# Optimization experiments

Hardware: AMD Instinct MI355X
Metric: run time of the kernel (lower is better)

## Reference

```python
import jax, jax.numpy as jnp
import numpy as np

B, N, E_PER_G = 32, 2048, 16384
NF, NHID, NCLS = 128, 128, 10
RATIO = 0.5
NT = B * N
E = B * E_PER_G
K1 = int(np.ceil(RATIO * N))        # 1024 nodes kept per graph after pool1
K2 = int(np.ceil(RATIO * K1))       # 512
K3 = int(np.ceil(RATIO * K2))       # 256


def setup_inputs() -> dict:
    key = jax.random.key(0)
    ks = jax.random.split(key, 16)
    x = jax.random.normal(ks[0], (NT, NF), dtype=jnp.float32)
    off = (jnp.arange(B, dtype=jnp.int32) * N)[:, None]
    src = (jax.random.randint(ks[1], (B, E_PER_G), 0, N, dtype=jnp.int32) + off).reshape(-1)
    dst = (jax.random.randint(ks[2], (B, E_PER_G), 0, N, dtype=jnp.int32) + off).reshape(-1)
    edge_index = jnp.stack([src, dst])
    batch = jnp.repeat(jnp.arange(B, dtype=jnp.int32), N)
    def lin(k, i, o):
        return jax.random.normal(k, (i, o), jnp.float32) / np.float32(np.sqrt(i))
    return {
        'x': x, 'edge_index': edge_index, 'batch': batch,
        'W1': lin(ks[3], NF, NHID), 'b1': jnp.zeros((NHID,), jnp.float32),
        'Wp1': lin(ks[4], NHID, 1), 'bp1': jnp.zeros((1,), jnp.float32),
        'W2': lin(ks[5], NHID, NHID), 'b2': jnp.zeros((NHID,), jnp.float32),
        'Wp2': lin(ks[6], NHID, 1), 'bp2': jnp.zeros((1,), jnp.float32),
        'W3': lin(ks[7], NHID, NHID), 'b3': jnp.zeros((NHID,), jnp.float32),
        'Wp3': lin(ks[8], NHID, 1), 'bp3': jnp.zeros((1,), jnp.float32),
        'lin1_W': lin(ks[9], 2 * NHID, NHID), 'lin1_b': jnp.zeros((NHID,), jnp.float32),
        'lin2_W': lin(ks[10], NHID, NHID // 2), 'lin2_b': jnp.zeros((NHID // 2,), jnp.float32),
        'lin3_W': lin(ks[11], NHID // 2, NCLS), 'lin3_b': jnp.zeros((NCLS,), jnp.float32),
    }


def gcn(x, src, dst, emask, nmask, W, b):
    # PyG GCNConv: add self-loops, symmetric normalization D^-1/2 (A+I) D^-1/2 @ (x W) + b.
    # Removed nodes/edges carry weight 0 via masks (equivalent to filter_adj re-indexing).
    h = x @ W
    deg = jnp.zeros((NT,), h.dtype).at[dst].add(emask) + nmask
    dinv = jnp.where(deg > 0, 1.0, 0.0) * jax.lax.rsqrt(jnp.where(deg > 0, deg, 1.0))
    coef = dinv[src] * dinv[dst] * emask               # [E]
    out = jnp.zeros_like(h).at[dst].add(coef[:, None] * h[src])
    out = out + ((dinv * dinv) * nmask)[:, None] * h   # self-loop term, norm = 1/deg
    return out + b


def sagpool(x, src, dst, emask, nmask, Wp, bp, k):
    # score = GCNConv(nhid,1); keep top-k per graph; x <- x[perm] * tanh(score[perm])
    score = gcn(x, src, dst, emask, nmask, Wp, bp)[:, 0]          # [NT]
    s = jnp.where(nmask > 0, score, -jnp.inf).reshape(B, N)
    _, idx = jax.lax.top_k(s, k)                                   # [B, k]
    keep = jnp.zeros((B, N), x.dtype).at[jnp.arange(B)[:, None], idx].set(1.0).reshape(-1)
    x_new = x * jnp.tanh(score)[:, None] * keep[:, None]
    emask_new = emask * keep[src] * keep[dst]                      # filter_adj
    return x_new, emask_new, keep


def readout(x, nmask, count):
    # [global_max_pool, global_mean_pool] over active nodes of each graph
    xb = x.reshape(B, N, -1)
    m = nmask.reshape(B, N, 1)
    mx = jnp.max(jnp.where(m > 0, xb, -jnp.inf), axis=1)
    mn = jnp.sum(xb * m, axis=1) / count
    return jnp.concatenate([mx, mn], axis=-1)


def reference(x, edge_index, batch, W1, b1, Wp1, bp1, W2, b2, Wp2, bp2,
              W3, b3, Wp3, bp3, lin1_W, lin1_b, lin2_W, lin2_b, lin3_W, lin3_b):
    src, dst = edge_index[0], edge_index[1]
    emask = jnp.ones((E,), x.dtype)
    nmask = jnp.ones((NT,), x.dtype)

    h = jax.nn.relu(gcn(x, src, dst, emask, nmask, W1, b1))
    h, emask, nmask = sagpool(h, src, dst, emask, nmask, Wp1, bp1, K1)
    x1 = readout(h, nmask, jnp.asarray(K1, x.dtype))

    h = jax.nn.relu(gcn(h, src, dst, emask, nmask, W2, b2))
    h, emask, nmask = sagpool(h, src, dst, emask, nmask, Wp2, bp2, K2)
    x2 = readout(h, nmask, jnp.asarray(K2, x.dtype))

    h = jax.nn.relu(gcn(h, src, dst, emask, nmask, W3, b3))
    h, emask, nmask = sagpool(h, src, dst, emask, nmask, Wp3, bp3, K3)
    x3 = readout(h, nmask, jnp.asarray(K3, x.dtype))

    g = x1 + x2 + x3
    g = jax.nn.relu(g @ lin1_W + lin1_b)   # dropout = identity in eval
    g = jax.nn.relu(g @ lin2_W + lin2_b)
    return jax.nn.log_softmax(g @ lin3_W + lin3_b, axis=-1)
```

## Files before the change

kernel.cpp:

```cpp
#include <hip/hip_runtime.h>
#include <math.h>


namespace {

constexpr int B_  = 32;
constexpr int N_  = 2048;
constexpr int NT  = B_ * N_;
constexpr int EPG = 16384;
constexpr int E_  = B_ * EPG;
constexpr int NCLS = 10;
constexpr int AST = 132;

__device__ __forceinline__ int relabel(int bid, int bpgsh) {
  int x = bid & 7, slot = bid >> 3;
  int g = x + 8 * (slot >> bpgsh);
  return (g << bpgsh) + (slot & ((1 << bpgsh) - 1));
}

__device__ void csr_build(const int* __restrict__ src, const int* __restrict__ dst,
                          int* __restrict__ off, int* __restrict__ srcp,
                          float* __restrict__ dinv, float* __restrict__ ds,
                          float* __restrict__ sws, int* hist) {
  const int g = blockIdx.x;
  const int t = threadIdx.x;
  const int base_n = g * N_;
  const int base_e = g * EPG;
  int* wsum4 = hist + 2048;
#pragma unroll
  for (int i = 0; i < 8; ++i) hist[t + 256 * i] = 0;
  __syncthreads();
  for (int i = 0; i < EPG / 256; i += 8) {
    int dd[8];
#pragma unroll
    for (int j = 0; j < 8; ++j) dd[j] = dst[base_e + t + 256 * (i + j)];
#pragma unroll
    for (int j = 0; j < 8; ++j) atomicAdd(&hist[dd[j] - base_n], 1);
  }
  __syncthreads();
  int a[8], ssum = 0;
#pragma unroll
  for (int i = 0; i < 8; ++i) { a[i] = hist[8 * t + i]; ssum += a[i]; }
  {
    int lane = t & 63, w = t >> 6;
    int v = ssum;
#pragma unroll
    for (int o = 1; o < 64; o <<= 1) {
      int nv = __shfl_up(v, o);
      if (lane >= o) v += nv;
    }
    if (lane == 63) wsum4[w] = v;
    __syncthreads();
    if (t == 0) {
      int accv = 0;
      for (int i = 0; i < 4; ++i) { int tmp = wsum4[i]; wsum4[i] = accv; accv += tmp; }
    }
    __syncthreads();
    int run = wsum4[w] + v - ssum;
#pragma unroll
    for (int i = 0; i < 8; ++i) {
      int n = 8 * t + i;
      off[base_n + n] = base_e + run;
      hist[n] = run;
      float d0 = 1.f + (float)a[i];
      float di0 = 1.f / sqrtf(d0);
      dinv[base_n + n] = di0;
      ds[base_n + n] = di0;
      sws[base_n + n] = di0 * di0;
      run += a[i];
    }
    if (g == B_ - 1 && t == 0) off[NT] = E_;
  }
  __syncthreads();
  for (int i = 0; i < EPG / 256; i += 8) {
    int dd[8], ss[8];
#pragma unroll
    for (int j = 0; j < 8; ++j) {
      int e = base_e + t + 256 * (i + j);
      dd[j] = dst[e];
      ss[j] = src[e];
    }
#pragma unroll
    for (int j = 0; j < 8; ++j) {
      int slot = atomicAdd(&hist[dd[j] - base_n], 1);
      srcp[base_e + slot] = ss[j];
    }
  }
}

__global__ __launch_bounds__(256) void k_matmul(const float* __restrict__ A,
                                                const float* __restrict__ W,
                                                float* __restrict__ C,
                                                const int* __restrict__ kept,
                                                int kshift, int bpgsh,
                                                const float* __restrict__ scaleArr,
                                                float* __restrict__ pmx,
                                                float* __restrict__ psm,
                                                const int* __restrict__ src,
                                                const int* __restrict__ dst,
                                                int* __restrict__ off,
                                                int* __restrict__ srcp,
                                                float* __restrict__ dinvW,
                                                float* __restrict__ dsW,
                                                float* __restrict__ swsW,
                                                int csrBlocks) {
  __shared__ float Ast[2][32 * AST];
  __shared__ float Ws[2][32 * 128];
  __shared__ int rowid[128];
  __shared__ float rsc[128];
  if ((int)blockIdx.x < csrBlocks) {
    csr_build(src, dst, off, srcp, dinvW, dsW, swsW, (int*)&Ast[0][0]);
    return;
  }
  const int tid = threadIdx.x;
  const int tile = relabel((int)blockIdx.x - csrBlocks, bpgsh);
  if (kept) {
    if (tid < 128) {
      int q = tile * 128 + tid;
      int g = q >> kshift;
      int row = kept[g * N_ + (q - (g << kshift))];
      rowid[tid] = row;
      rsc[tid] = scaleArr[row];
    }
    __syncthreads();
  }
  const int rowq = tid >> 4;
  const int colq = tid & 15;
  float4 va[4], vw[4];
#pragma unroll
  for (int i = 0; i < 4; ++i) {
    int idx = tid + 256 * i;
    int row = idx >> 3, f4 = idx & 7;
    int grw = kept ? rowid[row] : tile * 128 + row;
    va[i] = *(const float4*)&A[(size_t)grw * 128 + 4 * f4];
  }
#pragma unroll
  for (int i = 0; i < 4; ++i) {
    int idx = tid + 256 * i;
    int kk = idx >> 5, cf = idx & 31;
    vw[i] = *(const float4*)&W[(size_t)kk * 128 + 4 * cf];
  }
#pragma unroll
  for (int i = 0; i < 4; ++i) {
    int idx = tid + 256 * i;
    int row = idx >> 3, f4 = idx & 7;
    Ast[0][(4 * f4 + 0) * AST + row] = va[i].x;
    Ast[0][(4 * f4 + 1) * AST + row] = va[i].y;
    Ast[0][(4 * f4 + 2) * AST + row] = va[i].z;
    Ast[0][(4 * f4 + 3) * AST + row] = va[i].w;
  }
#pragma unroll
  for (int i = 0; i < 4; ++i) {
    int idx = tid + 256 * i;
    int kk = idx >> 5, cf = idx & 31;
    *(float4*)&Ws[0][kk * 128 + 4 * cf] = vw[i];
  }
  __syncthreads();
  float acc[8][8] = {};
  for (int c = 0; c < 4; ++c) {
    int cur = c & 1;
    if (c < 3) {
      int k0n = 32 * (c + 1);
#pragma unroll
      for (int i = 0; i < 4; ++i) {
        int idx = tid + 256 * i;
        int row = idx >> 3, f4 = idx & 7;
        int grw = kept ? rowid[row] : tile * 128 + row;
        va[i] = *(const float4*)&A[(size_t)grw * 128 + k0n + 4 * f4];
      }
#pragma unroll
      for (int i = 0; i < 4; ++i) {
        int idx = tid + 256 * i;
        int kk = idx >> 5, cf = idx & 31;
        vw[i] = *(const float4*)&W[(size_t)(k0n + kk) * 128 + 4 * cf];
      }
    }
#pragma unroll 2
    for (int kk = 0; kk < 32; ++kk) {
      float4 a0 = *(const float4*)&Ast[cur][kk * AST + 8 * rowq];
      float4 a1 = *(const float4*)&Ast[cur][kk * AST + 8 * rowq + 4];
      float4 w0 = *(const float4*)&Ws[cur][kk * 128 + 4 * colq];
      float4 w1 = *(const float4*)&Ws[cur][kk * 128 + 64 + 4 * colq];
      float a[8] = {a0.x, a0.y, a0.z, a0.w, a1.x, a1.y, a1.z, a1.w};
      float w[8] = {w0.x, w0.y, w0.z, w0.w, w1.x, w1.y, w1.z, w1.w};
#pragma unroll
      for (int r = 0; r < 8; ++r)
#pragma unroll
        for (int cc = 0; cc < 8; ++cc) acc[r][cc] += a[r] * w[cc];
    }
    if (kept) {
      int kkf = tid >> 3;
      int r0 = (tid & 7) * 16;
      float mxv = -INFINITY, smv = 0.f;
#pragma unroll
      for (int rr = 0; rr < 16; rr += 4) {
        float4 av = *(const float4*)&Ast[cur][kkf * AST + r0 + rr];
        float4 s4 = *(const float4*)&rsc[r0 + rr];
        float v0 = av.x * s4.x, v1 = av.y * s4.y;
        float v2 = av.z * s4.z, v3 = av.w * s4.w;
        mxv = fmaxf(fmaxf(fmaxf(mxv, v0), fmaxf(v1, v2)), v3);
        smv += v0 + v1 + v2 + v3;
      }
#pragma unroll
      for (int o = 4; o >= 1; o >>= 1) {
        mxv = fmaxf(mxv, __shfl_down(mxv, o));
        smv += __shfl_down(smv, o);
      }
      if ((tid & 7) == 0) {
        pmx[(size_t)tile * 128 + 32 * c + kkf] = mxv;
        psm[(size_t)tile * 128 + 32 * c + kkf] = smv;
      }
    }
    if (c < 3) {
      int nxt = cur ^ 1;
#pragma unroll
      for (int i = 0; i < 4; ++i) {
        int idx = tid + 256 * i;
        int row = idx >> 3, f4 = idx & 7;
        Ast[nxt][(4 * f4 + 0) * AST + row] = va[i].x;
        Ast[nxt][(4 * f4 + 1) * AST + row] = va[i].y;
        Ast[nxt][(4 * f4 + 2) * AST + row] = va[i].z;
        Ast[nxt][(4 * f4 + 3) * AST + row] = va[i].w;
      }
#pragma unroll
      for (int i = 0; i < 4; ++i) {
        int idx = tid + 256 * i;
        int kk = idx >> 5, cf = idx & 31;
        *(float4*)&Ws[nxt][kk * 128 + 4 * cf] = vw[i];
      }
      __syncthreads();
    }
  }
#pragma unroll
  for (int r = 0; r < 8; ++r) {
    int grw = kept ? rowid[8 * rowq + r] : tile * 128 + 8 * rowq + r;
    float* Crow = &C[(size_t)grw * 128];
    *(float4*)&Crow[4 * colq] = make_float4(acc[r][0], acc[r][1], acc[r][2], acc[r][3]);
    *(float4*)&Crow[64 + 4 * colq] = make_float4(acc[r][4], acc[r][5], acc[r][6], acc[r][7]);
  }
}

__global__ __launch_bounds__(256) void k_agg(const float4* __restrict__ t4,
                                             const int* __restrict__ off,
                                             const int* __restrict__ srcp,
                                             const float* __restrict__ dinv,
                                             const float* __restrict__ ds,
                                             const float* __restrict__ sws,
                                             const float* __restrict__ bias,
                                             const float* __restrict__ Wp,
                                             float4* __restrict__ h4,
                                             float* __restrict__ t1,
                                             const int* __restrict__ kept,
                                             int kshift, int bpgsh) {
  int q = relabel(blockIdx.x, bpgsh) * 8 + (threadIdx.x >> 5);
  int node;
  if (kept) {
    int g = q >> kshift;
    node = kept[g * N_ + (q - (g << kshift))];
  } else {
    node = q;
  }
  const int lane = threadIdx.x & 31;
  const float dvi = dinv[node];
  float sw = sws[node];
  float4 self = t4[(size_t)node * 32 + lane];
  float4 acc = make_float4(sw * self.x, sw * self.y, sw * self.z, sw * self.w);
  int s = off[node], en = off[node + 1];
  int j = s;
  for (; j + 8 <= en; j += 8) {
    int sv[8];
    float cv[8];
#pragma unroll
    for (int i = 0; i < 8; ++i) sv[i] = srcp[j + i];
#pragma unroll
    for (int i = 0; i < 8; ++i) cv[i] = ds[sv[i]] * dvi;
#pragma unroll
    for (int i = 0; i < 8; ++i) {
      if (cv[i] != 0.f) {
        float4 r = t4[(size_t)sv[i] * 32 + lane];
        acc.x += cv[i] * r.x; acc.y += cv[i] * r.y;
        acc.z += cv[i] * r.z; acc.w += cv[i] * r.w;
      }
    }
  }
  for (; j < en; ++j) {
    int s0 = srcp[j];
    float c0 = ds[s0] * dvi;
    if (c0 != 0.f) {
      float4 r0 = t4[(size_t)s0 * 32 + lane];
      acc.x += c0 * r0.x; acc.y += c0 * r0.y; acc.z += c0 * r0.z; acc.w += c0 * r0.w;
    }
  }
  float4 b4 = ((const float4*)bias)[lane];
  acc.x = fmaxf(acc.x + b4.x, 0.f);
  acc.y = fmaxf(acc.y + b4.y, 0.f);
  acc.z = fmaxf(acc.z + b4.z, 0.f);
  acc.w = fmaxf(acc.w + b4.w, 0.f);
  h4[(size_t)node * 32 + lane] = acc;
  float4 wp = ((const float4*)Wp)[lane];
  float part = acc.x * wp.x + acc.y * wp.y + acc.z * wp.z + acc.w * wp.w;
#pragma unroll
  for (int o = 16; o > 0; o >>= 1) part += __shfl_down(part, o, 32);
  if (lane == 0) t1[node] = part;
}

__global__ __launch_bounds__(1024) void k_pool(const float* __restrict__ t1,
                                               const int* __restrict__ off,
                                               const int* __restrict__ srcp,
                                               float* __restrict__ dinv,
                                               float* __restrict__ ds,
                                               float* __restrict__ sws,
                                               float* __restrict__ scale,
                                               const float* __restrict__ bp,
                                               int* __restrict__ kept,
                                               const float4* __restrict__ h4,
                                               float invk, int k,
                                               const int* __restrict__ inKept, int klen,
                                               const float* __restrict__ pmxA,
                                               const float* __restrict__ psmA,
                                               const float* __restrict__ pmxB,
                                               const float* __restrict__ psmB,
                                               const float* __restrict__ hW1,
                                               const float* __restrict__ hb1,
                                               const float* __restrict__ hW2,
                                               const float* __restrict__ hb2,
                                               const float* __restrict__ hW3,
                                               const float* __restrict__ hb3,
                                               float* __restrict__ out) {
  __shared__ float st1[2048];
  __shared__ float sdv[2048];
  __shared__ float skp[2048];
  __shared__ int skept[1024];
  __shared__ unsigned rephist[4096];
  __shared__ unsigned ebits[64];
  __shared__ int wsum[16];
  __shared__ unsigned bc_digit, bc_prev;
  __shared__ float gr[256], o1[128], o2[64], o3[NCLS];
  const int g = (blockIdx.x & 7) + 8 * (blockIdx.x >> 3);
  const int t = threadIdx.x;
  const int base = g * N_;
  st1[t] = t1[base + t];
  st1[t + 1024] = t1[base + t + 1024];
  sdv[t] = dinv[base + t];
  sdv[t + 1024] = dinv[base + t + 1024];
  skp[t] = 0.f;
  skp[t + 1024] = 0.f;
  if (t < 64) ebits[t] = 0u;
#pragma unroll
  for (int i = 0; i < 4; ++i) rephist[t + 1024 * i] = 0u;
  __syncthreads();
  int nodeq[2] = {-1, -1};
  float raw[2] = {0.f, 0.f};
  unsigned key[2] = {0xFFFFFFFFu, 0xFFFFFFFFu};
  float bpv = bp[0];
#pragma unroll
  for (int q = 0; q < 2; ++q) {
    int i = t + q * 1024;
    if (i >= klen) continue;
    int n = inKept ? (inKept[base + i] - base) : i;
    nodeq[q] = n;
    float di = sdv[n];
    float a = 0.f;
    int s = off[base + n], en = off[base + n + 1];
    int j = s;
    for (; j + 8 <= en; j += 8) {
      int sv[8];
#pragma unroll
      for (int i2 = 0; i2 < 8; ++i2) sv[i2] = srcp[j + i2] - base;
#pragma unroll
      for (int i2 = 0; i2 < 8; ++i2) a += sdv[sv[i2]] * st1[sv[i2]];
    }
    for (; j < en; ++j) {
      int sl = srcp[j] - base;
      a += sdv[sl] * st1[sl];
    }
    raw[q] = di * di * st1[n] + di * a + bpv;
    unsigned u = __float_as_uint(raw[q]);
    u = (u & 0x80000000u) ? ~u : (u | 0x80000000u);
    u = ~u;
    if (di <= 0.f) u = 0xFFFFFFFFu;
    key[q] = u;
  }
  unsigned prefix = 0u, rem = (unsigned)k;
  const int wv = t >> 6;
  for (int shift = 24; shift >= 0; shift -= 8) {
    unsigned mask = (shift == 24) ? 0u : (0xFFFFFFFFu << (shift + 8));
#pragma unroll
    for (int q = 0; q < 2; ++q)
      if (nodeq[q] >= 0 && (key[q] & mask) == prefix)
        atomicAdd(&rephist[(wv << 8) + ((key[q] >> shift) & 255u)], 1u);
    __syncthreads();
    unsigned binv = 0u, v = 0u;
    if (t < 256) {
#pragma unroll
      for (int w = 0; w < 16; ++w) binv += rephist[(w << 8) + t];
      v = binv;
#pragma unroll
      for (int o = 1; o < 64; o <<= 1) {
        unsigned nv = __shfl_up(v, o);
        if ((t & 63) >= o) v += nv;
      }
      if ((t & 63) == 63) wsum[t >> 6] = (int)v;
    }
    __syncthreads();
    if (t < 256) {
      unsigned pre = 0u;
      int w4 = t >> 6;
      for (int u = 0; u < w4; ++u) pre += (unsigned)wsum[u];
      unsigned inc = v + pre, exc = inc - binv;
      if (inc >= rem && exc < rem) { bc_digit = (unsigned)t; bc_prev = exc; }
    }
    __syncthreads();
    if (shift > 0) {
#pragma unroll
      for (int i = 0; i < 4; ++i) rephist[t + 1024 * i] = 0u;
    }
    __syncthreads();
    prefix |= bc_digit << shift;
    rem -= bc_prev;
  }
  const unsigned Tkey = prefix;
  const int need = (int)rem;
#pragma unroll
  for (int q = 0; q < 2; ++q) {
    int n = nodeq[q];
    if (n >= 0 && key[q] == Tkey) atomicOr(&ebits[n >> 5], 1u << (n & 31));
  }
  __syncthreads();
#pragma unroll
  for (int q = 0; q < 2; ++q) {
    int n = nodeq[q];
    if (n < 0) continue;
    float kp;
    if (key[q] < Tkey) {
      kp = 1.f;
    } else if (key[q] == Tkey) {
      int w = n >> 5;
      int rank = __popc(ebits[w] & ((1u << (n & 31)) - 1u));
      for (int u = 0; u < w; ++u) rank += __popc(ebits[u]);
      kp = (rank < need) ? 1.f : 0.f;
    } else {
      kp = 0.f;
    }
    skp[n] = kp;
    float sc = kp * tanhf(raw[q]);
    st1[n] = sc;
    scale[base + n] = sc;
  }
  __syncthreads();
  {
    int lane = t & 63, w = t >> 6;
    int a0 = (int)skp[2 * t], a1 = (int)skp[2 * t + 1];
    int ps = a0 + a1;
    int v = ps;
#pragma unroll
    for (int o = 1; o < 64; o <<= 1) {
      int nv = __shfl_up(v, o);
      if (lane >= o) v += nv;
    }
    if (lane == 63) wsum[w] = v;
    __syncthreads();
    if (t == 0) {
      int accv = 0;
      for (int i = 0; i < 16; ++i) { int tmp = wsum[i]; wsum[i] = accv; accv += tmp; }
    }
    __syncthreads();
    int excl = wsum[w] + v - ps;
    if (a0) { kept[base + excl] = base + 2 * t; skept[excl] = base + 2 * t; }
    if (a1) { kept[base + excl + a0] = base + 2 * t + 1; skept[excl + a0] = base + 2 * t + 1; }
  }
#pragma unroll
  for (int q = 0; q < 2; ++q) {
    int n = nodeq[q];
    if (n < 0) continue;
    float nm = skp[n];
    float d = nm;
    int s = off[base + n], en = off[base + n + 1];
    int j = s;
    for (; j + 8 <= en; j += 8) {
      int sv[8];
#pragma unroll
      for (int i2 = 0; i2 < 8; ++i2) sv[i2] = srcp[j + i2] - base;
#pragma unroll
      for (int i2 = 0; i2 < 8; ++i2) d += skp[sv[i2]];
    }
    for (; j < en; ++j) d += skp[srcp[j] - base];
    float di = (nm > 0.f) ? (1.f / sqrtf(d)) : 0.f;
    float sc = st1[n];
    dinv[base + n] = di;
    ds[base + n] = di * sc;
    sws[base + n] = di * di * sc;
  }
  if (!out) return;
  __syncthreads();
  const int lane = t & 31, ng = t >> 5;
  float4 mx = make_float4(-INFINITY, -INFINITY, -INFINITY, -INFINITY);
  float4 sm = make_float4(0.f, 0.f, 0.f, 0.f);
  for (int i = ng; i < k; i += 32) {
    int node = skept[i];
    float sc = st1[node - base];
    float4 v = h4[(size_t)node * 32 + lane];
    v.x *= sc; v.y *= sc; v.z *= sc; v.w *= sc;
    mx.x = fmaxf(mx.x, v.x); mx.y = fmaxf(mx.y, v.y);
    mx.z = fmaxf(mx.z, v.z); mx.w = fmaxf(mx.w, v.w);
    sm.x += v.x; sm.y += v.y; sm.z += v.z; sm.w += v.w;
  }
  float4* red = (float4*)rephist;
  for (int d = 16; d >= 1; d >>= 1) {
    if (ng >= d && ng < 2 * d) {
      red[(ng - d) * 32 + lane] = mx;
      red[512 + (ng - d) * 32 + lane] = sm;
    }
    __syncthreads();
    if (ng < d) {
      float4 omx = red[ng * 32 + lane];
      float4 osm = red[512 + ng * 32 + lane];
      mx.x = fmaxf(mx.x, omx.x); mx.y = fmaxf(mx.y, omx.y);
      mx.z = fmaxf(mx.z, omx.z); mx.w = fmaxf(mx.w, omx.w);
      sm.x += osm.x; sm.y += osm.y; sm.z += osm.z; sm.w += osm.w;
    }
    __syncthreads();
  }
  if (ng == 0) {
    gr[4 * lane + 0] = mx.x;
    gr[4 * lane + 1] = mx.y;
    gr[4 * lane + 2] = mx.z;
    gr[4 * lane + 3] = mx.w;
    gr[128 + 4 * lane + 0] = sm.x * invk;
    gr[128 + 4 * lane + 1] = sm.y * invk;
    gr[128 + 4 * lane + 2] = sm.z * invk;
    gr[128 + 4 * lane + 3] = sm.w * invk;
  }
  __syncthreads();
  if (t < 128) {
    float mxA = -INFINITY, smA = 0.f;
#pragma unroll
    for (int p = 0; p < 8; ++p) {
      mxA = fmaxf(mxA, pmxA[(size_t)(g * 8 + p) * 128 + t]);
      smA += psmA[(size_t)(g * 8 + p) * 128 + t];
    }
    float mxB = -INFINITY, smB = 0.f;
#pragma unroll
    for (int p = 0; p < 4; ++p) {
      mxB = fmaxf(mxB, pmxB[(size_t)(g * 4 + p) * 128 + t]);
      smB += psmB[(size_t)(g * 4 + p) * 128 + t];
    }
    gr[t] += mxA + mxB;
    gr[t + 128] += smA * (1.f / 1024.f) + smB * (1.f / 512.f);
  }
  __syncthreads();
  if (t < 128) {
    float a = hb1[t];
    for (int kk = 0; kk < 256; ++kk) a += gr[kk] * hW1[kk * 128 + t];
    o1[t] = fmaxf(a, 0.f);
  }
  __syncthreads();
  if (t < 64) {
    float a2 = hb2[t];
    for (int kk = 0; kk < 128; ++kk) a2 += o1[kk] * hW2[kk * 64 + t];
    o2[t] = fmaxf(a2, 0.f);
  }
  __syncthreads();
  if (t < NCLS) {
    float a3 = hb3[t];
    for (int kk = 0; kk < 64; ++kk) a3 += o2[kk] * hW3[kk * NCLS + t];
    o3[t] = a3;
  }
  __syncthreads();
  if (t == 0) {
    float m = -INFINITY;
    for (int c = 0; c < NCLS; ++c) m = fmaxf(m, o3[c]);
    float sum = 0.f;
    for (int c = 0; c < NCLS; ++c) sum += expf(o3[c] - m);
    float lse = logf(sum);
    for (int c = 0; c < NCLS; ++c) out[g * NCLS + c] = o3[c] - m - lse;
  }
}

}

extern "C" void kernel_launch(void* const* d_in, const int* in_sizes, int n_in,
                              void* d_out, int out_size, void* d_ws, size_t ws_size,
                              hipStream_t stream) {
  const float* x = (const float*)d_in[0];
  const int* ei = (const int*)d_in[1];
  const int* src = ei;
  const int* dst = ei + E_;
  const float* Wl[3]  = {(const float*)d_in[3], (const float*)d_in[7], (const float*)d_in[11]};
  const float* bl[3]  = {(const float*)d_in[4], (const float*)d_in[8], (const float*)d_in[12]};
  const float* Wpl[3] = {(const float*)d_in[5], (const float*)d_in[9], (const float*)d_in[13]};
  const float* bpl[3] = {(const float*)d_in[6], (const float*)d_in[10], (const float*)d_in[14]};
  const float* l1W = (const float*)d_in[15];
  const float* l1b = (const float*)d_in[16];
  const float* l2W = (const float*)d_in[17];
  const float* l2b = (const float*)d_in[18];
  const float* l3W = (const float*)d_in[19];
  const float* l3b = (const float*)d_in[20];

  char* p = (char*)d_ws;
  auto alloc = [&](size_t bytes) -> void* {
    void* r = (void*)p;
    p += (bytes + 255) & ~size_t(255);
    return r;
  };
  float* h      = (float*)alloc((size_t)NT * 128 * 4);
  float* t      = (float*)alloc((size_t)NT * 128 * 4);
  float* dinv   = (float*)alloc(NT * 4);
  float* ds     = (float*)alloc(NT * 4);
  float* sws    = (float*)alloc(NT * 4);
  float* scale  = (float*)alloc(NT * 4);
  float* t1     = (float*)alloc(NT * 4);
  int*   srcp   = (int*)alloc(E_ * 4);
  int*   off    = (int*)alloc((NT + 1) * 4);
  int*   kept0  = (int*)alloc(NT * 4);
  int*   kept1  = (int*)alloc(NT * 4);
  int*   kept2  = (int*)alloc(NT * 4);
  float* pmxA   = (float*)alloc(256 * 128 * 4);
  float* psmA   = (float*)alloc(256 * 128 * 4);
  float* pmxB   = (float*)alloc(128 * 128 * 4);
  float* psmB   = (float*)alloc(128 * 128 * 4);

  int* keptL[3] = {kept0, kept1, kept2};
  const int K[3] = {1024, 512, 256};
  const int KSH[3] = {10, 9, 8};
  float* pmxL[3] = {nullptr, pmxA, pmxB};
  float* psmL[3] = {nullptr, psmA, psmB};

  const float* inF = x;
  for (int l = 0; l < 3; ++l) {
    const int* inKept = (l == 0) ? nullptr : keptL[l - 1];
    int inKsh = (l == 0) ? 11 : KSH[l - 1];
    int nrows = (l == 0) ? NT : B_ * K[l - 1];
    int mm_bpgsh = (l == 0) ? 4 : (l == 1 ? 3 : 2);
    int ag_bpgsh = (l == 0) ? 8 : (l == 1 ? 7 : 6);
    int csrB = (l == 0) ? B_ : 0;
    int klen = (l == 0) ? N_ : K[l - 1];
    bool last = (l == 2);
    k_matmul<<<nrows / 128 + csrB, 256, 0, stream>>>(
        inF, Wl[l], t, inKept, inKsh, mm_bpgsh, scale, pmxL[l], psmL[l],
        src, dst, off, srcp, dinv, ds, sws, csrB);
    k_agg<<<nrows / 8, 256, 0, stream>>>((const float4*)t, off, srcp, dinv, ds, sws,
                                         bl[l], Wpl[l], (float4*)h, t1, inKept, inKsh,
                                         ag_bpgsh);
    k_pool<<<B_, 1024, 0, stream>>>(t1, off, srcp, dinv, ds, sws, scale, bpl[l],
                                    keptL[l], (const float4*)h,
                                    1.f / (float)K[l], K[l], inKept, klen,
                                    last ? pmxA : nullptr, last ? psmA : nullptr,
                                    last ? pmxB : nullptr, last ? psmB : nullptr,
                                    l1W, l1b, l2W, l2b, l3W, l3b,
                                    last ? (float*)d_out : nullptr);
    inF = h;
  }
}
```

Before: 299.1 us.

## Enlarge matmul tile to 256 rows with 8x16 per-thread accumulators, single-buffered LDS

The dense feature transform now processes 256 rows per block instead of 128, and each thread computes an 8x16 output micro-tile, raising arithmetic intensity per shared-memory load. LDS double-buffering is dropped in favour of a single buffer guarded by an extra barrier, and the W tile gets a padded stride. The per-column readout partials are computed in two halves so they keep the 128-row granularity. The change halves the block count and raises register pressure, which may reduce occupancy and overlap.

```diff
diff --git a/kernel.cpp b/kernel.cpp
--- a/kernel.cpp
+++ b/kernel.cpp
@@ -10,7 +10,8 @@
 constexpr int EPG = 16384;
 constexpr int E_  = B_ * EPG;
 constexpr int NCLS = 10;
-constexpr int AST = 132;
+constexpr int AST = 260;
+constexpr int WST = 132;
 
 __device__ __forceinline__ int relabel(int bid, int bpgsh) {
   int x = bid & 7, slot = bid >> 3;
@@ -104,34 +105,32 @@
                                                 float* __restrict__ dsW,
                                                 float* __restrict__ swsW,
                                                 int csrBlocks) {
-  __shared__ float Ast[2][32 * AST];
-  __shared__ float Ws[2][32 * 128];
-  __shared__ int rowid[128];
-  __shared__ float rsc[128];
+  __shared__ float Ast[32 * AST];
+  __shared__ float Ws[32 * WST];
+  __shared__ int rowid[256];
+  __shared__ float rsc[256];
   if ((int)blockIdx.x < csrBlocks) {
-    csr_build(src, dst, off, srcp, dinvW, dsW, swsW, (int*)&Ast[0][0]);
+    csr_build(src, dst, off, srcp, dinvW, dsW, swsW, (int*)&Ast[0]);
     return;
   }
   const int tid = threadIdx.x;
   const int tile = relabel((int)blockIdx.x - csrBlocks, bpgsh);
   if (kept) {
-    if (tid < 128) {
-      int q = tile * 128 + tid;
-      int g = q >> kshift;
-      int row = kept[g * N_ + (q - (g << kshift))];
-      rowid[tid] = row;
-      rsc[tid] = scaleArr[row];
-    }
-    __syncthreads();
-  }
-  const int rowq = tid >> 4;
-  const int colq = tid & 15;
-  float4 va[4], vw[4];
-#pragma unroll
-  for (int i = 0; i < 4; ++i) {
+    int q = tile * 256 + tid;
+    int g = q >> kshift;
+    int row = kept[g * N_ + (q - (g << kshift))];
+    rowid[tid] = row;
+    rsc[tid] = scaleArr[row];
+    __syncthreads();
+  }
+  const int rowq = tid >> 3;
+  const int colq = tid & 7;
+  float4 va[8], vw[4];
+#pragma unroll
+  for (int i = 0; i < 8; ++i) {
     int idx = tid + 256 * i;
     int row = idx >> 3, f4 = idx & 7;
-    int grw = kept ? rowid[row] : tile * 128 + row;
+    int grw = kept ? rowid[row] : tile * 256 + row;
     va[i] = *(const float4*)&A[(size_t)grw * 128 + 4 * f4];
   }
 #pragma unroll
@@ -141,31 +140,30 @@
     vw[i] = *(const float4*)&W[(size_t)kk * 128 + 4 * cf];
   }
 #pragma unroll
-  for (int i = 0; i < 4; ++i) {
+  for (int i = 0; i < 8; ++i) {
     int idx = tid + 256 * i;
     int row = idx >> 3, f4 = idx & 7;
-    Ast[0][(4 * f4 + 0) * AST + row] = va[i].x;
-    Ast[0][(4 * f4 + 1) * AST + row] = va[i].y;
-    Ast[0][(4 * f4 + 2) * AST + row] = va[i].z;
-    Ast[0][(4 * f4 + 3) * AST + row] = va[i].w;
+    Ast[(4 * f4 + 0) * AST + row] = va[i].x;
+    Ast[(4 * f4 + 1) * AST + row] = va[i].y;
+    Ast[(4 * f4 + 2) * AST + row] = va[i].z;
+    Ast[(4 * f4 + 3) * AST + row] = va[i].w;
   }
 #pragma unroll
   for (int i = 0; i < 4; ++i) {
     int idx = tid + 256 * i;
     int kk = idx >> 5, cf = idx & 31;
-    *(float4*)&Ws[0][kk * 128 + 4 * cf] = vw[i];
-  }
-  __syncthreads();
-  float acc[8][8] = {};
+    *(float4*)&Ws[kk * WST + 4 * cf] = vw[i];
+  }
+  __syncthreads();
+  float acc[8][16] = {};
   for (int c = 0; c < 4; ++c) {
-    int cur = c & 1;
     if (c < 3) {
       int k0n = 32 * (c + 1);
 #pragma unroll
-      for (int i = 0; i < 4; ++i) {
+      for (int i = 0; i < 8; ++i) {
         int idx = tid + 256 * i;
         int row = idx >> 3, f4 = idx & 7;
-        int grw = kept ? rowid[row] : tile * 128 + row;
+        int grw = kept ? rowid[row] : tile * 256 + row;
         va[i] = *(const float4*)&A[(size_t)grw * 128 + k0n + 4 * f4];
       }
 #pragma unroll
@@ -177,66 +175,77 @@
     }
 #pragma unroll 2
     for (int kk = 0; kk < 32; ++kk) {
-      float4 a0 = *(const float4*)&Ast[cur][kk * AST + 8 * rowq];
-      float4 a1 = *(const float4*)&Ast[cur][kk * AST + 8 * rowq + 4];
-      float4 w0 = *(const float4*)&Ws[cur][kk * 128 + 4 * colq];
-      float4 w1 = *(const float4*)&Ws[cur][kk * 128 + 64 + 4 * colq];
+      float4 a0 = *(const float4*)&Ast[kk * AST + 4 * rowq];
+      float4 a1 = *(const float4*)&Ast[kk * AST + 128 + 4 * rowq];
+      float4 w0 = *(const float4*)&Ws[kk * WST + 4 * colq];
+      float4 w1 = *(const float4*)&Ws[kk * WST + 32 + 4 * colq];
+      float4 w2 = *(const float4*)&Ws[kk * WST + 64 + 4 * colq];
+      float4 w3 = *(const float4*)&Ws[kk * WST + 96 + 4 * colq];
       float a[8] = {a0.x, a0.y, a0.z, a0.w, a1.x, a1.y, a1.z, a1.w};
-      float w[8] = {w0.x, w0.y, w0.z, w0.w, w1.x, w1.y, w1.z, w1.w};
+      float w[16] = {w0.x, w0.y, w0.z, w0.w, w1.x, w1.y, w1.z, w1.w,
+                     w2.x, w2.y, w2.z, w2.w, w3.x, w3.y, w3.z, w3.w};
 #pragma unroll
       for (int r = 0; r < 8; ++r)
 #pragma unroll
-        for (int cc = 0; cc < 8; ++cc) acc[r][cc] += a[r] * w[cc];
+        for (int cc = 0; cc < 16; ++cc) acc[r][cc] += a[r] * w[cc];
     }
     if (kept) {
       int kkf = tid >> 3;
-      int r0 = (tid & 7) * 16;
-      float mxv = -INFINITY, smv = 0.f;
-#pragma unroll
-      for (int rr = 0; rr < 16; rr += 4) {
-        float4 av = *(const float4*)&Ast[cur][kkf * AST + r0 + rr];
-        float4 s4 = *(const float4*)&rsc[r0 + rr];
-        float v0 = av.x * s4.x, v1 = av.y * s4.y;
-        float v2 = av.z * s4.z, v3 = av.w * s4.w;
-        mxv = fmaxf(fmaxf(fmaxf(mxv, v0), fmaxf(v1, v2)), v3);
-        smv += v0 + v1 + v2 + v3;
+      int sub = tid & 7;
+#pragma unroll
+      for (int half = 0; half < 2; ++half) {
+        int r0 = half * 128 + sub * 16;
+        float mxv = -INFINITY, smv = 0.f;
+#pragma unroll
+        for (int rr = 0; rr < 16; rr += 4) {
+          float4 av = *(const float4*)&Ast[kkf * AST + r0 + rr];
+          float4 s4 = *(const float4*)&rsc[r0 + rr];
+          float v0 = av.x * s4.x, v1 = av.y * s4.y;
+          float v2 = av.z * s4.z, v3 = av.w * s4.w;
+          mxv = fmaxf(fmaxf(fmaxf(mxv, v0), fmaxf(v1, v2)), v3);
+          smv += v0 + v1 + v2 + v3;
+        }
+#pragma unroll
+        for (int o = 4; o >= 1; o >>= 1) {
+          mxv = fmaxf(mxv, __shfl_down(mxv, o, 8));
+          smv += __shfl_down(smv, o, 8);
+        }
+        if (sub == 0) {
+          pmx[(size_t)(2 * tile + half) * 128 + 32 * c + kkf] = mxv;
+          psm[(size_t)(2 * tile + half) * 128 + 32 * c + kkf] = smv;
+        }
       }
-#pragma unroll
-      for (int o = 4; o >= 1; o >>= 1) {
-        mxv = fmaxf(mxv, __shfl_down(mxv, o));
-        smv += __shfl_down(smv, o);
-      }
-      if ((tid & 7) == 0) {
-        pmx[(size_t)tile * 128 + 32 * c + kkf] = mxv;
-        psm[(size_t)tile * 128 + 32 * c + kkf] = smv;
-      }
     }
     if (c < 3) {
-      int nxt = cur ^ 1;
-#pragma unroll
-      for (int i = 0; i < 4; ++i) {
+      __syncthreads();
+#pragma unroll
+      for (int i = 0; i < 8; ++i) {
         int idx = tid + 256 * i;
         int row = idx >> 3, f4 = idx & 7;
-        Ast[nxt][(4 * f4 + 0) * AST + row] = va[i].x;
-        Ast[nxt][(4 * f4 + 1) * AST + row] = va[i].y;
-        Ast[nxt][(4 * f4 + 2) * AST + row] = va[i].z;
-        Ast[nxt][(4 * f4 + 3) * AST + row] = va[i].w;
+        Ast[(4 * f4 + 0) * AST + row] = va[i].x;
+        Ast[(4 * f4 + 1) * AST + row] = va[i].y;
+        Ast[(4 * f4 + 2) * AST + row] = va[i].z;
+        Ast[(4 * f4 + 3) * AST + row] = va[i].w;
       }
 #pragma unroll
       for (int i = 0; i < 4; ++i) {
         int idx = tid + 256 * i;
         int kk = idx >> 5, cf = idx & 31;
-        *(float4*)&Ws[nxt][kk * 128 + 4 * cf] = vw[i];
+        *(float4*)&Ws[kk * WST + 4 * cf] = vw[i];
       }
       __syncthreads();
     }
   }
 #pragma unroll
   for (int r = 0; r < 8; ++r) {
-    int grw = kept ? rowid[8 * rowq + r] : tile * 128 + 8 * rowq + r;
+    int lrow = (r < 4) ? (4 * rowq + r) : (128 + 4 * rowq + (r - 4));
+    int grw = kept ? rowid[lrow] : tile * 256 + lrow;
     float* Crow = &C[(size_t)grw * 128];
-    *(float4*)&Crow[4 * colq] = make_float4(acc[r][0], acc[r][1], acc[r][2], acc[r][3]);
-    *(float4*)&Crow[64 + 4 * colq] = make_float4(acc[r][4], acc[r][5], acc[r][6], acc[r][7]);
+#pragma unroll
+    for (int w = 0; w < 4; ++w)
+      *(float4*)&Crow[4 * colq + 32 * w] =
+          make_float4(acc[r][4 * w + 0], acc[r][4 * w + 1],
+                      acc[r][4 * w + 2], acc[r][4 * w + 3]);
   }
 }
 
@@ -631,12 +640,12 @@
     const int* inKept = (l == 0) ? nullptr : keptL[l - 1];
     int inKsh = (l == 0) ? 11 : KSH[l - 1];
     int nrows = (l == 0) ? NT : B_ * K[l - 1];
-    int mm_bpgsh = (l == 0) ? 4 : (l == 1 ? 3 : 2);
+    int mm_bpgsh = (l == 0) ? 3 : (l == 1 ? 2 : 1);
     int ag_bpgsh = (l == 0) ? 8 : (l == 1 ? 7 : 6);
     int csrB = (l == 0) ? B_ : 0;
     int klen = (l == 0) ? N_ : K[l - 1];
     bool last = (l == 2);
-    k_matmul<<<nrows / 128 + csrB, 256, 0, stream>>>(
+    k_matmul<<<nrows / 256 + csrB, 256, 0, stream>>>(
         inF, Wl[l], t, inKept, inKsh, mm_bpgsh, scale, pmxL[l], psmL[l],
         src, dst, off, srcp, dinv, ds, sws, csrB);
     k_agg<<<nrows / 8, 256, 0, stream>>>((const float4*)t, off, srcp, dinv, ds, sws,
```

After: 374.7 us. 25.3% more time.
